# Kernel optimization log

Measured on AMD Instinct MI355X. Metric: run time of the kernel, lower is better.

The kernel has to match this reference:

```python
import jax, jax.numpy as jnp
import numpy as np

N_NODES = 4096
N_EDGES = 524288
IN_DIM = 6
EMB_N = 4
EMB_D = 8
EDGE_D = 1
HID = 64
N_HEADS = 4
LN_EPS = 1e-5


def _layernorm(h, g, b):
    m = jnp.mean(h, axis=-1, keepdims=True)
    v = jnp.mean(jnp.square(h - m), axis=-1, keepdims=True)
    return (h - m) * jax.lax.rsqrt(v + LN_EPS) * g + b


def setup_inputs() -> dict:
    key = jax.random.key(0)
    ks = jax.random.split(key, 16)
    s = lambda fan_in: 1.0 / np.sqrt(fan_in)
    inp = {
        'x': jax.random.normal(ks[0], (N_NODES, IN_DIM), jnp.float32),
        'edge_attr': jax.random.uniform(ks[1], (N_EDGES, EDGE_D), jnp.float32),
        'entity_emb': jax.random.normal(ks[2], (EMB_N, EMB_D), jnp.float32),
        'lin1_w': jax.random.uniform(ks[3], (HID, IN_DIM + EMB_D + EDGE_D), jnp.float32, -s(15), s(15)),
        'lin1_b': jnp.zeros((HID,), jnp.float32),
        'lay_w': jax.random.uniform(ks[4], (HID, HID), jnp.float32, -s(HID), s(HID)),
        'lay_b': jnp.zeros((HID,), jnp.float32),
        'ln_g': jnp.ones((HID,), jnp.float32),
        'ln_b': jnp.zeros((HID,), jnp.float32),
        'in_proj_w': jax.random.uniform(ks[5], (3 * HID, HID), jnp.float32, -s(HID), s(HID)),
        'in_proj_b': jnp.zeros((3 * HID,), jnp.float32),
        'out_proj_w': jax.random.uniform(ks[6], (HID, HID), jnp.float32, -s(HID), s(HID)),
        'out_proj_b': jnp.zeros((HID,), jnp.float32),
        'an_g': jnp.ones((HID,), jnp.float32),
        'an_b': jnp.zeros((HID,), jnp.float32),
        'out_w': jax.random.uniform(ks[7], (HID, HID), jnp.float32, -s(HID), s(HID)),
        'out_b': jnp.zeros((HID,), jnp.float32),
        'edge_index': jax.random.randint(ks[8], (2, N_EDGES), 0, N_NODES, jnp.int64),
        'entity_type': jax.random.randint(ks[9], (N_NODES,), 0, EMB_N, jnp.int64),
    }
    return inp


def reference(x, edge_attr, entity_emb, lin1_w, lin1_b, lay_w, lay_b, ln_g, ln_b,
              in_proj_w, in_proj_b, out_proj_w, out_proj_b, an_g, an_b, out_w, out_b,
              edge_index, entity_type):
    # --- EmbedConv ---
    # concat node features with entity embedding: [N, 6+8]
    xe = jnp.concatenate([x, entity_emb[entity_type]], axis=-1)
    src, dst = edge_index[0], edge_index[1]
    # gather source nodes + edge attr: [E, 15]
    msg = jnp.concatenate([xe[src], edge_attr], axis=-1)
    msg = _layernorm(jax.nn.relu(msg @ lin1_w.T + lin1_b), ln_g, ln_b)
    # layer_N = 1 extra layer, shared LayerNorm
    msg = _layernorm(jax.nn.relu(msg @ lay_w.T + lay_b), ln_g, ln_b)
    # scatter-add aggregate into destination nodes: [N, 64]
    h = jax.ops.segment_sum(msg, dst, num_segments=N_NODES)
    # --- MultiheadAttention over all nodes as one sequence (eval: no dropout) ---
    qkv = h @ in_proj_w.T + in_proj_b  # [N, 3H]
    q, k, v = jnp.split(qkv, 3, axis=-1)
    hd = HID // N_HEADS
    q = q.reshape(N_NODES, N_HEADS, hd).transpose(1, 0, 2)  # [h, n, d]
    k = k.reshape(N_NODES, N_HEADS, hd).transpose(1, 0, 2)
    v = v.reshape(N_NODES, N_HEADS, hd).transpose(1, 0, 2)
    scores = jnp.einsum('hnd,hmd->hnm', q, k) / np.sqrt(hd)
    attn = jax.nn.softmax(scores, axis=-1)
    o = jnp.einsum('hnm,hmd->hnd', attn, v).transpose(1, 0, 2).reshape(N_NODES, HID)
    o = o @ out_proj_w.T + out_proj_b
    h = _layernorm(h + o, an_g, an_b)
    # --- output layer ---
    return h @ out_w.T + out_b
```

## Files before the change

kernel.cpp:

```cpp
#include <hip/hip_runtime.h>

#define N_NODES 4096
#define N_EDGES 524288
#define HID 64

typedef short short8 __attribute__((ext_vector_type(8)));
typedef float f32x4 __attribute__((ext_vector_type(4)));

__device__ __forceinline__ float bcastf(float v, int l) {
    return __int_as_float(__builtin_amdgcn_readlane(__float_as_int(v), l));
}

__device__ __forceinline__ void wave_sum2(float& a, float& b) {
    #pragma unroll
    for (int off = 32; off > 0; off >>= 1) {
        a += __shfl_xor(a, off, 64);
        b += __shfl_xor(b, off, 64);
    }
}

__device__ __forceinline__ short f2bf(float f) {
    unsigned u = __float_as_uint(f);
    u = u + 0x7FFFu + ((u >> 16) & 1u);
    return (short)(u >> 16);
}
__device__ __forceinline__ float bf2f(short s) {
    return __uint_as_float(((unsigned)(unsigned short)s) << 16);
}
__device__ __forceinline__ void split_cheap(float f, short& hi, short& lo) {
    unsigned u = __float_as_uint(f);
    unsigned hb = u & 0xffff0000u;
    float lof = f - __uint_as_float(hb);
    hi = (short)(u >> 16);
    lo = (short)(__float_as_uint(lof) >> 16);
}

__global__ void xe_hist_wprep(const float* __restrict__ x, const float* __restrict__ emb,
                              const int* __restrict__ etype, const int* __restrict__ ei,
                              const float* __restrict__ w1, const float* __restrict__ w2,
                              const float* __restrict__ ipw,
                              unsigned short* __restrict__ xh, unsigned short* __restrict__ xl,
                              int* __restrict__ cnt, int* __restrict__ rank,
                              unsigned short* __restrict__ w1fh, unsigned short* __restrict__ w1fl,
                              unsigned short* __restrict__ w2fh, unsigned short* __restrict__ w2fl,
                              unsigned short* __restrict__ ipfh, unsigned short* __restrict__ ipfl) {
    int tid = blockIdx.x * 256 + threadIdx.x;
    int d = ei[N_EDGES + tid];
    rank[tid] = atomicAdd(&cnt[d], 1);
    if (tid < N_NODES * 16) {
        int n = tid >> 4, i = tid & 15;
        float v = 0.f;
        if (i < 6) v = x[n * 6 + i];
        else if (i < 14) v = emb[etype[n] * 8 + (i - 6)];
        short hi = f2bf(v);
        short lo = f2bf(v - bf2f(hi));
        xh[tid] = (unsigned short)hi;
        xl[tid] = (unsigned short)lo;
    }
    if (tid < 2048) {
        int g = tid >> 9, ln = (tid >> 3) & 63, j = tid & 7;
        int mm = ln & 15, qq = ln >> 4;
        int k = qq * 8 + j;
        float w = (k < 15) ? w1[(g * 16 + mm) * 15 + k] : 0.f;
        short hi = f2bf(w);
        w1fh[tid] = (unsigned short)hi;
        w1fl[tid] = (unsigned short)f2bf(w - bf2f(hi));
    }
    if (tid < 4096) {
        int idx = tid >> 9, ln = (tid >> 3) & 63, j = tid & 7;
        int mm = ln & 15, qq = ln >> 4;
        int g = idx >> 1, tt = idx & 1;
        float w = w2[(g * 16 + mm) * 64 + tt * 32 + qq * 8 + j];
        short hi = f2bf(w);
        w2fh[tid] = (unsigned short)hi;
        w2fl[tid] = (unsigned short)f2bf(w - bf2f(hi));
    }
    if (tid < 12288) {
        int idx = tid >> 9, ln = (tid >> 3) & 63, j = tid & 7;
        int mm = ln & 15, qq = ln >> 4;
        int og = idx >> 1, tt = idx & 1;
        float w = ipw[(og * 16 + mm) * 64 + tt * 32 + qq * 8 + j];
        short hi = f2bf(w);
        ipfh[tid] = (unsigned short)hi;
        ipfl[tid] = (unsigned short)f2bf(w - bf2f(hi));
    }
}

__global__ void __launch_bounds__(256) scatter_scan(
        const int* __restrict__ cnt, const int* __restrict__ ei,
        const float* __restrict__ edge_attr, const int* __restrict__ rank,
        int* __restrict__ bnd,
        int* __restrict__ ssrc, float* __restrict__ sea) {
    __shared__ int lbnd[4096];
    __shared__ int wsum[4];
    int t = threadIdx.x;
    int base = t * 16;
    int v16[16];
    int T = 0;
    #pragma unroll
    for (int j = 0; j < 16; j++) { v16[j] = cnt[base + j]; T += v16[j]; }
    int inc = T;
    int l = t & 63;
    #pragma unroll
    for (int off = 1; off < 64; off <<= 1) {
        int v = __shfl_up(inc, off, 64);
        if (l >= off) inc += v;
    }
    if (l == 63) wsum[t >> 6] = inc;
    __syncthreads();
    int wo = 0;
    for (int w = 0; w < (t >> 6); w++) wo += wsum[w];
    int run = wo + inc - T;
    #pragma unroll
    for (int j = 0; j < 16; j++) {
        lbnd[base + j] = run;
        run += v16[j];
    }
    if (blockIdx.x == 0) {
        #pragma unroll
        for (int j = 0; j < 16; j++) bnd[base + j] = lbnd[base + j];
        if (t == 255) bnd[4096] = run;
    }
    __syncthreads();
    int e = blockIdx.x * 256 + t;
    int d = ei[N_EDGES + e];
    int pos = lbnd[d] + rank[e];
    ssrc[pos] = ei[e];
    sea[pos] = edge_attr[e];
}

__global__ void __launch_bounds__(256) edge_gather_mfma(
        const unsigned short* __restrict__ xh, const unsigned short* __restrict__ xl,
        const int* __restrict__ ssrc, const float* __restrict__ sea,
        const int* __restrict__ bnd,
        const unsigned short* __restrict__ w1fh, const unsigned short* __restrict__ w1fl,
        const unsigned short* __restrict__ w2fh, const unsigned short* __restrict__ w2fl,
        const float* __restrict__ w1, const float* __restrict__ b1,
        const float* __restrict__ b2,
        const float* __restrict__ lg, const float* __restrict__ lb,
        float* __restrict__ h) {
    __shared__ float Y[4][16 * 68];
    __shared__ float hpart[4][64];
    int lane = threadIdx.x & 63;
    int wv = threadIdx.x >> 6;
    int m = lane & 15;
    int q = lane >> 4;
    float* Yw = Y[wv];

    short8 b1h[4], b1l[4], b2h[8], b2l[8];
    #pragma unroll
    for (int g = 0; g < 4; g++) {
        b1h[g] = *(const short8*)(w1fh + (g * 64 + lane) * 8);
        b1l[g] = *(const short8*)(w1fl + (g * 64 + lane) * 8);
    }
    #pragma unroll
    for (int idx = 0; idx < 8; idx++) {
        b2h[idx] = *(const short8*)(w2fh + (idx * 64 + lane) * 8);
        b2l[idx] = *(const short8*)(w2fl + (idx * 64 + lane) * 8);
    }
    float w14[4], b1v[4], b2v[4], gam[4], bet[4];
    #pragma unroll
    for (int g = 0; g < 4; g++) {
        int row = g * 16 + m;
        w14[g] = w1[row * 15 + 14];
        b1v[g] = b1[row];
        b2v[g] = b2[row];
        gam[g] = lg[row];
        bet[g] = lb[row];
    }

    int node = blockIdx.x * 2 + (wv >> 1);
    int hf = wv & 1;
    int start = bnd[node], end = bnd[node + 1];
    int ntiles = (end - start + 15) >> 4;
    int h0 = (ntiles + 1) >> 1;
    int tcnt = hf ? (ntiles - h0) : h0;
    int astart = start + (hf ? h0 : 0) * 16;
    float acc[4] = {0.f, 0.f, 0.f, 0.f};

    for (int t = 0; t < tcnt; t++) {
        int base = astart + t * 16;
        int e = base + m;
        int srcn = ssrc[(e < end) ? e : (end - 1)];
        short8 a1h = (short8)0, a1l = (short8)0;
        if (q < 2) {
            a1h = *(const short8*)(xh + srcn * 16 + q * 8);
            a1l = *(const short8*)(xl + srcn * 16 + q * 8);
        }
        float ea[4];
        #pragma unroll
        for (int i = 0; i < 4; i++) {
            int idx = base + q * 4 + i;
            ea[i] = (idx < end) ? sea[idx] : 0.f;
        }
        f32x4 c1[4];
        #pragma unroll
        for (int g = 0; g < 4; g++) {
            f32x4 c = {0.f, 0.f, 0.f, 0.f};
            c = __builtin_amdgcn_mfma_f32_16x16x32_bf16(a1l, b1h[g], c, 0, 0, 0);
            c = __builtin_amdgcn_mfma_f32_16x16x32_bf16(a1h, b1l[g], c, 0, 0, 0);
            c = __builtin_amdgcn_mfma_f32_16x16x32_bf16(a1h, b1h[g], c, 0, 0, 0);
            c1[g] = c;
        }
        float s[4] = {0, 0, 0, 0}, s2[4] = {0, 0, 0, 0};
        float t1[4][4];
        #pragma unroll
        for (int g = 0; g < 4; g++) {
            #pragma unroll
            for (int i = 0; i < 4; i++) {
                float v = c1[g][i] + b1v[g] + w14[g] * ea[i];
                v = fmaxf(v, 0.f);
                t1[g][i] = v;
                s[i] += v;
                s2[i] += v * v;
            }
        }
        #pragma unroll
        for (int off = 1; off < 16; off <<= 1) {
            #pragma unroll
            for (int i = 0; i < 4; i++) {
                s[i] += __shfl_xor(s[i], off, 64);
                s2[i] += __shfl_xor(s2[i], off, 64);
            }
        }
        #pragma unroll
        for (int i = 0; i < 4; i++) {
            float mean = s[i] * (1.f / 64.f);
            float var = s2[i] * (1.f / 64.f) - mean * mean;
            s[i] = mean;
            s2[i] = rsqrtf(var + 1e-5f);
        }
        #pragma unroll
        for (int g = 0; g < 4; g++) {
            #pragma unroll
            for (int i = 0; i < 4; i++) {
                float y = (t1[g][i] - s[i]) * s2[i] * gam[g] + bet[g];
                Yw[(q * 4 + i) * 68 + g * 16 + m] = y;
            }
        }
        short8 a2h[2], a2l[2];
        #pragma unroll
        for (int t2 = 0; t2 < 2; t2++) {
            #pragma unroll
            for (int j = 0; j < 8; j++) {
                float v = Yw[m * 68 + t2 * 32 + q * 8 + j];
                short hi, lo;
                split_cheap(v, hi, lo);
                a2h[t2][j] = hi;
                a2l[t2][j] = lo;
            }
        }
        float s_[4] = {0, 0, 0, 0}, s2_[4] = {0, 0, 0, 0};
        float t2v[4][4];
        #pragma unroll
        for (int g = 0; g < 4; g++) {
            f32x4 c = {0.f, 0.f, 0.f, 0.f};
            #pragma unroll
            for (int t2 = 0; t2 < 2; t2++) {
                c = __builtin_amdgcn_mfma_f32_16x16x32_bf16(a2l[t2], b2h[g * 2 + t2], c, 0, 0, 0);
                c = __builtin_amdgcn_mfma_f32_16x16x32_bf16(a2h[t2], b2l[g * 2 + t2], c, 0, 0, 0);
                c = __builtin_amdgcn_mfma_f32_16x16x32_bf16(a2h[t2], b2h[g * 2 + t2], c, 0, 0, 0);
            }
            #pragma unroll
            for (int i = 0; i < 4; i++) {
                float v = c[i] + b2v[g];
                v = fmaxf(v, 0.f);
                t2v[g][i] = v;
                s_[i] += v;
                s2_[i] += v * v;
            }
        }
        #pragma unroll
        for (int off = 1; off < 16; off <<= 1) {
            #pragma unroll
            for (int i = 0; i < 4; i++) {
                s_[i] += __shfl_xor(s_[i], off, 64);
                s2_[i] += __shfl_xor(s2_[i], off, 64);
            }
        }
        #pragma unroll
        for (int i = 0; i < 4; i++) {
            float mean = s_[i] * (1.f / 64.f);
            float var = s2_[i] * (1.f / 64.f) - mean * mean;
            float rs = rsqrtf(var + 1e-5f);
            bool valid = (base + q * 4 + i) < end;
            #pragma unroll
            for (int g = 0; g < 4; g++) {
                float z = (t2v[g][i] - mean) * rs * gam[g] + bet[g];
                if (valid) acc[g] += z;
            }
        }
    }
    #pragma unroll
    for (int g = 0; g < 4; g++) {
        acc[g] += __shfl_xor(acc[g], 16, 64);
        acc[g] += __shfl_xor(acc[g], 32, 64);
    }
    float a01 = (q & 1) ? acc[1] : acc[0];
    float a23 = (q & 1) ? acc[3] : acc[2];
    float av = (q & 2) ? a23 : a01;
    hpart[wv][q * 16 + m] = av;
    __syncthreads();
    if (threadIdx.x < 128) {
        int nn = threadIdx.x >> 6, f = threadIdx.x & 63;
        h[(blockIdx.x * 2 + nn) * 64 + f] = hpart[2 * nn][f] + hpart[2 * nn + 1][f];
    }
}

__global__ void __launch_bounds__(256) qkv_mfma(
        const float* __restrict__ h, const float* __restrict__ b,
        const unsigned short* __restrict__ ipfh, const unsigned short* __restrict__ ipfl,
        unsigned short* __restrict__ qhp, unsigned short* __restrict__ qlp,
        unsigned short* __restrict__ khp, unsigned short* __restrict__ klp,
        unsigned short* __restrict__ vT) {
    int lane = threadIdx.x & 63;
    int wv = threadIdx.x >> 6;
    int m = lane & 15;
    int q = lane >> 4;
    int wid = blockIdx.x * 4 + wv;
    int tile = wid / 12;
    int og = wid - tile * 12;
    short8 bh[2], bl[2];
    #pragma unroll
    for (int t = 0; t < 2; t++) {
        bh[t] = *(const short8*)(ipfh + ((og * 2 + t) * 64 + lane) * 8);
        bl[t] = *(const short8*)(ipfl + ((og * 2 + t) * 64 + lane) * 8);
    }
    f32x4 c = {0.f, 0.f, 0.f, 0.f};
    #pragma unroll
    for (int t = 0; t < 2; t++) {
        const float* hr = h + (tile * 16 + m) * 64 + t * 32 + q * 8;
        float4 f0 = *(const float4*)hr;
        float4 f1 = *(const float4*)(hr + 4);
        float av8[8] = {f0.x, f0.y, f0.z, f0.w, f1.x, f1.y, f1.z, f1.w};
        short8 ah, al;
        #pragma unroll
        for (int j = 0; j < 8; j++) {
            short hi, lo;
            split_cheap(av8[j], hi, lo);
            ah[j] = hi;
            al[j] = lo;
        }
        c = __builtin_amdgcn_mfma_f32_16x16x32_bf16(al, bh[t], c, 0, 0, 0);
        c = __builtin_amdgcn_mfma_f32_16x16x32_bf16(ah, bl[t], c, 0, 0, 0);
        c = __builtin_amdgcn_mfma_f32_16x16x32_bf16(ah, bh[t], c, 0, 0, 0);
    }
    int o = og * 16 + m;
    float bias = b[o];
    #pragma unroll
    for (int r = 0; r < 4; r++) {
        int node = tile * 16 + q * 4 + r;
        float val = c[r] + bias;
        if (og < 4) {
            float aq = val * (0.25f * 1.44269504f);
            size_t idx = ((size_t)(og * N_NODES + node)) * 16 + m;
            short hi = f2bf(aq);
            qhp[idx] = (unsigned short)hi;
            qlp[idx] = (unsigned short)f2bf(aq - bf2f(hi));
        } else if (og < 8) {
            size_t idx = ((size_t)((og - 4) * N_NODES + node)) * 16 + m;
            short hi = f2bf(val);
            khp[idx] = (unsigned short)hi;
            klp[idx] = (unsigned short)f2bf(val - bf2f(hi));
        } else {
            int feat = (og - 8) * 16 + m;
            vT[(size_t)feat * N_NODES + node] = (unsigned short)f2bf(val);
        }
    }
}

__global__ void __launch_bounds__(256) attn_mfma(
        const unsigned short* __restrict__ qhp, const unsigned short* __restrict__ qlp,
        const unsigned short* __restrict__ khp, const unsigned short* __restrict__ klp,
        const unsigned short* __restrict__ vT,
        float* __restrict__ part_o, float* __restrict__ part_ml) {
    __shared__ unsigned short Pl[4][16 * 72];
    int lane = threadIdx.x & 63;
    int wv = threadIdx.x >> 6;
    int m = lane & 15;
    int g = lane >> 4;
    unsigned short* Pw = Pl[wv];
    const short8 vones = {0x3F80, 0x3F80, 0x3F80, 0x3F80, 0x3F80, 0x3F80, 0x3F80, 0x3F80};

    int wid = blockIdx.x * 4 + wv;
    int kc = wid & 7;
    int qt = (wid >> 3) & 255;
    int head = wid >> 11;

    short8 aqh = (short8)0, aql = (short8)0;
    if (g < 2) {
        size_t qi = ((size_t)(head * N_NODES + qt * 16 + m)) * 16 + g * 8;
        aqh = *(const short8*)(qhp + qi);
        aql = *(const short8*)(qlp + qi);
    }
    float mS[4], lS[4];
    #pragma unroll
    for (int r = 0; r < 4; r++) { mS[r] = -3e38f; lS[r] = 0.f; }
    f32x4 Ot = {0.f, 0.f, 0.f, 0.f};

    const unsigned short* khb = khp + (size_t)head * N_NODES * 16;
    const unsigned short* klb = klp + (size_t)head * N_NODES * 16;
    const unsigned short* vtb = vT + (size_t)(head * 16 + m) * N_NODES;

    for (int bblk = 0; bblk < 8; bblk++) {
        int n0 = kc * 512 + bblk * 64;
        f32x4 S[4];
        #pragma unroll
        for (int s = 0; s < 4; s++) {
            short8 bkh = (short8)0, bkl = (short8)0;
            if (g < 2) {
                size_t ki = ((size_t)(n0 + s * 16 + m)) * 16 + g * 8;
                bkh = *(const short8*)(khb + ki);
                bkl = *(const short8*)(klb + ki);
            }
            f32x4 c = {0.f, 0.f, 0.f, 0.f};
            c = __builtin_amdgcn_mfma_f32_16x16x32_bf16(aqh, bkl, c, 0, 0, 0);
            c = __builtin_amdgcn_mfma_f32_16x16x32_bf16(aql, bkh, c, 0, 0, 0);
            c = __builtin_amdgcn_mfma_f32_16x16x32_bf16(aqh, bkh, c, 0, 0, 0);
            S[s] = c;
        }
        float mr[4];
        #pragma unroll
        for (int r = 0; r < 4; r++)
            mr[r] = fmaxf(fmaxf(S[0][r], S[1][r]), fmaxf(S[2][r], S[3][r]));
        #pragma unroll
        for (int off = 1; off < 16; off <<= 1)
            #pragma unroll
            for (int r = 0; r < 4; r++) mr[r] = fmaxf(mr[r], __shfl_xor(mr[r], off, 64));
        float alpha[4];
        #pragma unroll
        for (int r = 0; r < 4; r++) {
            float mn = fmaxf(mS[r], mr[r]);
            alpha[r] = exp2f(mS[r] - mn);
            mS[r] = mn;
        }
        #pragma unroll
        for (int s = 0; s < 4; s++) {
            #pragma unroll
            for (int r = 0; r < 4; r++) {
                float p = exp2f(S[s][r] - mS[r]);
                Pw[(g * 4 + r) * 72 + s * 16 + m] = (unsigned short)f2bf(p);
            }
        }
        #pragma unroll
        for (int r = 0; r < 4; r++) lS[r] *= alpha[r];
        int sel = lane & 3;
        float a01 = (sel & 1) ? alpha[1] : alpha[0];
        float a23 = (sel & 1) ? alpha[3] : alpha[2];
        float aown = (sel & 2) ? a23 : a01;
        int srcl = ((m >> 2) << 4) | (m & 3);
        float ab = __int_as_float(__builtin_amdgcn_ds_bpermute(srcl << 2, __float_as_int(aown)));
        #pragma unroll
        for (int r = 0; r < 4; r++) Ot[r] *= ab;
        f32x4 cl = {0.f, 0.f, 0.f, 0.f};
        #pragma unroll
        for (int t = 0; t < 2; t++) {
            short8 avf = *(const short8*)(vtb + n0 + t * 32 + g * 8);
            short8 bpf = *(const short8*)(Pw + m * 72 + t * 32 + g * 8);
            cl = __builtin_amdgcn_mfma_f32_16x16x32_bf16(vones, bpf, cl, 0, 0, 0);
            Ot = __builtin_amdgcn_mfma_f32_16x16x32_bf16(avf, bpf, Ot, 0, 0, 0);
        }
        #pragma unroll
        for (int r = 0; r < 4; r++) {
            float rsum = __int_as_float(
                __builtin_amdgcn_ds_bpermute((g * 4 + r) << 2, __float_as_int(cl[0])));
            lS[r] += rsum;
        }
    }
    size_t pb = ((size_t)(head * 8 + kc) * 256 + qt) * 256;
    *(f32x4*)(part_o + pb + m * 16 + g * 4) = Ot;
    if (m == 0) {
        size_t mb = ((size_t)(head * 8 + kc) * 256 + qt) * 32;
        #pragma unroll
        for (int r = 0; r < 4; r++) {
            part_ml[mb + g * 4 + r] = mS[r];
            part_ml[mb + 16 + g * 4 + r] = lS[r];
        }
    }
}

__global__ void post_kernel(const float* __restrict__ h,
                            const float* __restrict__ part_o, const float* __restrict__ part_ml,
                            const float* __restrict__ opw, const float* __restrict__ opb,
                            const float* __restrict__ ag, const float* __restrict__ ab,
                            const float* __restrict__ ow, const float* __restrict__ ob,
                            float* __restrict__ out) {
    __shared__ float wl1[64 * 65];
    __shared__ float wl2[64 * 65];
    for (int i = threadIdx.x; i < 4096; i += blockDim.x) {
        int r = i >> 6, c = i & 63;
        wl1[r * 65 + c] = opw[i];
        wl2[r * 65 + c] = ow[i];
    }
    __syncthreads();
    int lane = threadIdx.x & 63;
    int n = blockIdx.x * 4 + (threadIdx.x >> 6);
    int j = lane;
    int head = j >> 4, d = j & 15;
    int qt = n >> 4, qi = n & 15;
    float M = -3e38f, L = 0.f, Ov = 0.f;
    #pragma unroll
    for (int c = 0; c < 8; c++) {
        size_t base = ((size_t)(head * 8 + c) * 256 + qt);
        float mc = part_ml[base * 32 + qi];
        float lc = part_ml[base * 32 + 16 + qi];
        float ov = part_o[base * 256 + qi * 16 + d];
        if (mc > M) {
            float sc = exp2f(M - mc);
            M = mc;
            L = L * sc + lc;
            Ov = Ov * sc + ov;
        } else {
            float sc = exp2f(mc - M);
            L = fmaf(lc, sc, L);
            Ov = fmaf(ov, sc, Ov);
        }
    }
    float oj = Ov / L;
    float acc = opb[j];
    #pragma unroll
    for (int k = 0; k < 64; k++) acc = fmaf(wl1[j * 65 + k], bcastf(oj, k), acc);
    float r = h[n * 64 + j] + acc;
    float s = r, s2 = r * r;
    wave_sum2(s, s2);
    float mean = s * (1.f / 64.f);
    float var = s2 * (1.f / 64.f) - mean * mean;
    float hn = (r - mean) * rsqrtf(var + 1e-5f) * ag[j] + ab[j];
    float acc2 = ob[j];
    #pragma unroll
    for (int k = 0; k < 64; k++) acc2 = fmaf(wl2[j * 65 + k], bcastf(hn, k), acc2);
    out[n * 64 + j] = acc2;
}

extern "C" void kernel_launch(void* const* d_in, const int* in_sizes, int n_in,
                              void* d_out, int out_size, void* d_ws, size_t ws_size,
                              hipStream_t stream) {
    const float* x        = (const float*)d_in[0];
    const float* edge_attr= (const float*)d_in[1];
    const float* emb      = (const float*)d_in[2];
    const float* lin1_w   = (const float*)d_in[3];
    const float* lin1_b   = (const float*)d_in[4];
    const float* lay_w    = (const float*)d_in[5];
    const float* lay_b    = (const float*)d_in[6];
    const float* ln_g     = (const float*)d_in[7];
    const float* ln_b     = (const float*)d_in[8];
    const float* ipw      = (const float*)d_in[9];
    const float* ipb      = (const float*)d_in[10];
    const float* opw      = (const float*)d_in[11];
    const float* opb      = (const float*)d_in[12];
    const float* ang      = (const float*)d_in[13];
    const float* anb      = (const float*)d_in[14];
    const float* ow       = (const float*)d_in[15];
    const float* ob       = (const float*)d_in[16];
    const int*   ei       = (const int*)d_in[17];
    const int*   et       = (const int*)d_in[18];

    char* wsb = (char*)d_ws;
    size_t off = 0;
    unsigned short* xe_hi = (unsigned short*)(wsb + off); off += 131072;
    unsigned short* xe_lo = (unsigned short*)(wsb + off); off += 131072;
    float* h              = (float*)(wsb + off);          off += 1048576;
    unsigned short* qhp   = (unsigned short*)(wsb + off); off += 524288;
    unsigned short* qlp   = (unsigned short*)(wsb + off); off += 524288;
    unsigned short* khp   = (unsigned short*)(wsb + off); off += 524288;
    unsigned short* klp   = (unsigned short*)(wsb + off); off += 524288;
    unsigned short* vT    = (unsigned short*)(wsb + off); off += 524288;
    float* part_o         = (float*)(wsb + off);          off += 8388608;
    float* part_ml        = (float*)(wsb + off);          off += 1048576;
    int*   cnt            = (int*)(wsb + off);            off += 16384;
    int*   bnd            = (int*)(wsb + off);            off += 16388;
    off = (off + 255) & ~(size_t)255;
    int*   rank           = (int*)(wsb + off);            off += 2097152;
    int*   ssrc           = (int*)(wsb + off);            off += 2097152;
    float* sea            = (float*)(wsb + off);          off += 2097152;
    unsigned short* w1fh  = (unsigned short*)(wsb + off); off += 4096;
    unsigned short* w1fl  = (unsigned short*)(wsb + off); off += 4096;
    unsigned short* w2fh  = (unsigned short*)(wsb + off); off += 8192;
    unsigned short* w2fl  = (unsigned short*)(wsb + off); off += 8192;
    unsigned short* ipfh  = (unsigned short*)(wsb + off); off += 24576;
    unsigned short* ipfl  = (unsigned short*)(wsb + off); off += 24576;

    (void)hipMemsetAsync(cnt, 0, 4096 * sizeof(int), stream);
    xe_hist_wprep<<<2048, 256, 0, stream>>>(x, emb, et, ei, lin1_w, lay_w, ipw,
                                            xe_hi, xe_lo, cnt, rank,
                                            w1fh, w1fl, w2fh, w2fl, ipfh, ipfl);
    scatter_scan<<<2048, 256, 0, stream>>>(cnt, ei, edge_attr, rank, bnd, ssrc, sea);
    edge_gather_mfma<<<2048, 256, 0, stream>>>(xe_hi, xe_lo, ssrc, sea, bnd,
                                               w1fh, w1fl, w2fh, w2fl,
                                               lin1_w, lin1_b, lay_b, ln_g, ln_b, h);
    qkv_mfma<<<768, 256, 0, stream>>>(h, ipb, ipfh, ipfl, qhp, qlp, khp, klp, vT);
    attn_mfma<<<2048, 256, 0, stream>>>(qhp, qlp, khp, klp, vT, part_o, part_ml);
    post_kernel<<<1024, 256, 0, stream>>>(h, part_o, part_ml, opw, opb, ang, anb, ow, ob,
                                          (float*)d_out);
}
```

Measured before the change: 270.5 us.

## Precompute per-node first-layer projection and fold LayerNorm affine into weights

The first linear layer's node-dependent part (x and entity embedding times lin1_w plus bias) is computed once per node into a float table A1. The per-edge kernel now only gathers that row, adds the edge-attr term and applies relu and LayerNorm in registers, removing the first MFMA stage and the LDS round-trip. LayerNorm gamma/beta are folded into the second-layer weights and bias, and the final gamma/beta are applied once per node after aggregation using the edge count. Each block now handles one node with four waves striding tiles, and the second-layer weights are staged in LDS. The cost is a larger per-edge gather (64 floats instead of 32 bf16 values) and fp32 rounding that differs slightly from the reference.

New measurement: 242.2 us. 1.12x faster.

```diff
diff --git a/kernel.cpp b/kernel.cpp
--- a/kernel.cpp
+++ b/kernel.cpp
@@ -35,42 +35,36 @@
     lo = (short)(__float_as_uint(lof) >> 16);
 }
 
-__global__ void xe_hist_wprep(const float* __restrict__ x, const float* __restrict__ emb,
-                              const int* __restrict__ etype, const int* __restrict__ ei,
-                              const float* __restrict__ w1, const float* __restrict__ w2,
-                              const float* __restrict__ ipw,
-                              unsigned short* __restrict__ xh, unsigned short* __restrict__ xl,
-                              int* __restrict__ cnt, int* __restrict__ rank,
-                              unsigned short* __restrict__ w1fh, unsigned short* __restrict__ w1fl,
-                              unsigned short* __restrict__ w2fh, unsigned short* __restrict__ w2fl,
-                              unsigned short* __restrict__ ipfh, unsigned short* __restrict__ ipfl) {
+__global__ void hist_prep(const float* __restrict__ x, const float* __restrict__ emb,
+                          const int* __restrict__ etype, const int* __restrict__ ei,
+                          const float* __restrict__ w1, const float* __restrict__ b1,
+                          const float* __restrict__ w2, const float* __restrict__ lng,
+                          const float* __restrict__ lnb, const float* __restrict__ b2,
+                          const float* __restrict__ ipw,
+                          float* __restrict__ A1, int* __restrict__ cnt, int* __restrict__ rank,
+                          unsigned short* __restrict__ w2fh, unsigned short* __restrict__ w2fl,
+                          unsigned short* __restrict__ ipfh, unsigned short* __restrict__ ipfl,
+                          float* __restrict__ b2p) {
     int tid = blockIdx.x * 256 + threadIdx.x;
     int d = ei[N_EDGES + tid];
     rank[tid] = atomicAdd(&cnt[d], 1);
-    if (tid < N_NODES * 16) {
-        int n = tid >> 4, i = tid & 15;
-        float v = 0.f;
-        if (i < 6) v = x[n * 6 + i];
-        else if (i < 14) v = emb[etype[n] * 8 + (i - 6)];
-        short hi = f2bf(v);
-        short lo = f2bf(v - bf2f(hi));
-        xh[tid] = (unsigned short)hi;
-        xl[tid] = (unsigned short)lo;
-    }
-    if (tid < 2048) {
-        int g = tid >> 9, ln = (tid >> 3) & 63, j = tid & 7;
-        int mm = ln & 15, qq = ln >> 4;
-        int k = qq * 8 + j;
-        float w = (k < 15) ? w1[(g * 16 + mm) * 15 + k] : 0.f;
-        short hi = f2bf(w);
-        w1fh[tid] = (unsigned short)hi;
-        w1fl[tid] = (unsigned short)f2bf(w - bf2f(hi));
+    if (tid < N_NODES * 64) {
+        int n = tid >> 6, f = tid & 63;
+        const float* wr = w1 + f * 15;
+        float acc = b1[f];
+        #pragma unroll
+        for (int k = 0; k < 6; k++) acc = fmaf(x[n * 6 + k], wr[k], acc);
+        int e = etype[n];
+        #pragma unroll
+        for (int k = 0; k < 8; k++) acc = fmaf(emb[e * 8 + k], wr[6 + k], acc);
+        A1[tid] = acc;
     }
     if (tid < 4096) {
         int idx = tid >> 9, ln = (tid >> 3) & 63, j = tid & 7;
         int mm = ln & 15, qq = ln >> 4;
         int g = idx >> 1, tt = idx & 1;
-        float w = w2[(g * 16 + mm) * 64 + tt * 32 + qq * 8 + j];
+        int col = tt * 32 + qq * 8 + j;
+        float w = w2[(g * 16 + mm) * 64 + col] * lng[col];
         short hi = f2bf(w);
         w2fh[tid] = (unsigned short)hi;
         w2fl[tid] = (unsigned short)f2bf(w - bf2f(hi));
@@ -83,6 +77,11 @@
         short hi = f2bf(w);
         ipfh[tid] = (unsigned short)hi;
         ipfl[tid] = (unsigned short)f2bf(w - bf2f(hi));
+    }
+    if (tid < 64) {
+        float acc = b2[tid];
+        for (int c = 0; c < 64; c++) acc = fmaf(w2[tid * 64 + c], lnb[c], acc);
+        b2p[tid] = acc;
     }
 }
 
@@ -129,164 +128,125 @@
     sea[pos] = edge_attr[e];
 }
 
-__global__ void __launch_bounds__(256) edge_gather_mfma(
-        const unsigned short* __restrict__ xh, const unsigned short* __restrict__ xl,
+__global__ void __launch_bounds__(256, 4) edge_gather_mfma(
+        const float* __restrict__ A1,
         const int* __restrict__ ssrc, const float* __restrict__ sea,
         const int* __restrict__ bnd,
-        const unsigned short* __restrict__ w1fh, const unsigned short* __restrict__ w1fl,
         const unsigned short* __restrict__ w2fh, const unsigned short* __restrict__ w2fl,
-        const float* __restrict__ w1, const float* __restrict__ b1,
-        const float* __restrict__ b2,
+        const float* __restrict__ w1, const float* __restrict__ b2p,
         const float* __restrict__ lg, const float* __restrict__ lb,
         float* __restrict__ h) {
-    __shared__ float Y[4][16 * 68];
+    __shared__ uint4 lw2h4[512];
+    __shared__ uint4 lw2l4[512];
     __shared__ float hpart[4][64];
-    int lane = threadIdx.x & 63;
-    int wv = threadIdx.x >> 6;
+    int tid = threadIdx.x;
+    {
+        const uint4* gh = (const uint4*)w2fh;
+        const uint4* gl = (const uint4*)w2fl;
+        lw2h4[tid] = gh[tid];
+        lw2h4[tid + 256] = gh[tid + 256];
+        lw2l4[tid] = gl[tid];
+        lw2l4[tid + 256] = gl[tid + 256];
+    }
+    const unsigned short* lw2h = (const unsigned short*)lw2h4;
+    const unsigned short* lw2l = (const unsigned short*)lw2l4;
+
+    int lane = tid & 63;
+    int wv = tid >> 6;
     int m = lane & 15;
     int q = lane >> 4;
-    float* Yw = Y[wv];
-
-    short8 b1h[4], b1l[4], b2h[8], b2l[8];
-    #pragma unroll
-    for (int g = 0; g < 4; g++) {
-        b1h[g] = *(const short8*)(w1fh + (g * 64 + lane) * 8);
-        b1l[g] = *(const short8*)(w1fl + (g * 64 + lane) * 8);
-    }
-    #pragma unroll
-    for (int idx = 0; idx < 8; idx++) {
-        b2h[idx] = *(const short8*)(w2fh + (idx * 64 + lane) * 8);
-        b2l[idx] = *(const short8*)(w2fl + (idx * 64 + lane) * 8);
-    }
-    float w14[4], b1v[4], b2v[4], gam[4], bet[4];
-    #pragma unroll
-    for (int g = 0; g < 4; g++) {
-        int row = g * 16 + m;
-        w14[g] = w1[row * 15 + 14];
-        b1v[g] = b1[row];
-        b2v[g] = b2[row];
-        gam[g] = lg[row];
-        bet[g] = lb[row];
-    }
-
-    int node = blockIdx.x * 2 + (wv >> 1);
-    int hf = wv & 1;
+
+    float w14f[16];
+    #pragma unroll
+    for (int t2 = 0; t2 < 2; t2++)
+        #pragma unroll
+        for (int j = 0; j < 8; j++)
+            w14f[t2 * 8 + j] = w1[(t2 * 32 + q * 8 + j) * 15 + 14];
+    float b2v[4];
+    #pragma unroll
+    for (int g = 0; g < 4; g++) b2v[g] = b2p[g * 16 + m];
+
+    int node = blockIdx.x;
     int start = bnd[node], end = bnd[node + 1];
     int ntiles = (end - start + 15) >> 4;
-    int h0 = (ntiles + 1) >> 1;
-    int tcnt = hf ? (ntiles - h0) : h0;
-    int astart = start + (hf ? h0 : 0) * 16;
     float acc[4] = {0.f, 0.f, 0.f, 0.f};
-
-    for (int t = 0; t < tcnt; t++) {
-        int base = astart + t * 16;
+    __syncthreads();
+
+    for (int t = wv; t < ntiles; t += 4) {
+        int base = start + t * 16;
         int e = base + m;
-        int srcn = ssrc[(e < end) ? e : (end - 1)];
-        short8 a1h = (short8)0, a1l = (short8)0;
-        if (q < 2) {
-            a1h = *(const short8*)(xh + srcn * 16 + q * 8);
-            a1l = *(const short8*)(xl + srcn * 16 + q * 8);
-        }
-        float ea[4];
-        #pragma unroll
-        for (int i = 0; i < 4; i++) {
-            int idx = base + q * 4 + i;
-            ea[i] = (idx < end) ? sea[idx] : 0.f;
-        }
-        f32x4 c1[4];
+        int ec = (e < end) ? e : (end - 1);
+        int srcn = ssrc[ec];
+        float eav = sea[ec];
+        const float* ar = A1 + srcn * 64 + q * 8;
+        float4 va = *(const float4*)(ar);
+        float4 vb = *(const float4*)(ar + 4);
+        float4 vc = *(const float4*)(ar + 32);
+        float4 vd = *(const float4*)(ar + 36);
+        float v[16] = {va.x, va.y, va.z, va.w, vb.x, vb.y, vb.z, vb.w,
+                       vc.x, vc.y, vc.z, vc.w, vd.x, vd.y, vd.z, vd.w};
+        float s = 0.f, s2 = 0.f;
+        #pragma unroll
+        for (int j = 0; j < 16; j++) {
+            float u = fmaxf(fmaf(w14f[j], eav, v[j]), 0.f);
+            v[j] = u;
+            s += u;
+            s2 = fmaf(u, u, s2);
+        }
+        s += __shfl_xor(s, 16, 64);  s2 += __shfl_xor(s2, 16, 64);
+        s += __shfl_xor(s, 32, 64);  s2 += __shfl_xor(s2, 32, 64);
+        float mean = s * (1.f / 64.f);
+        float var = s2 * (1.f / 64.f) - mean * mean;
+        float rs = rsqrtf(var + 1e-5f);
+        float a0 = -mean * rs;
+        short8 a2h[2], a2l[2];
+        #pragma unroll
+        for (int t2 = 0; t2 < 2; t2++)
+            #pragma unroll
+            for (int j = 0; j < 8; j++) {
+                short hi, lo;
+                split_cheap(fmaf(v[t2 * 8 + j], rs, a0), hi, lo);
+                a2h[t2][j] = hi;
+                a2l[t2][j] = lo;
+            }
+        int ob = (t >> 20);
+        float s_[4] = {0, 0, 0, 0}, s2_[4] = {0, 0, 0, 0};
+        float t2v[4][4];
         #pragma unroll
         for (int g = 0; g < 4; g++) {
             f32x4 c = {0.f, 0.f, 0.f, 0.f};
-            c = __builtin_amdgcn_mfma_f32_16x16x32_bf16(a1l, b1h[g], c, 0, 0, 0);
-            c = __builtin_amdgcn_mfma_f32_16x16x32_bf16(a1h, b1l[g], c, 0, 0, 0);
-            c = __builtin_amdgcn_mfma_f32_16x16x32_bf16(a1h, b1h[g], c, 0, 0, 0);
-            c1[g] = c;
-        }
-        float s[4] = {0, 0, 0, 0}, s2[4] = {0, 0, 0, 0};
-        float t1[4][4];
-        #pragma unroll
-        for (int g = 0; g < 4; g++) {
+            #pragma unroll
+            for (int t2 = 0; t2 < 2; t2++) {
+                short8 bh = *(const short8*)(lw2h + ((g * 2 + t2) * 64 + lane + ob) * 8);
+                short8 bl = *(const short8*)(lw2l + ((g * 2 + t2) * 64 + lane + ob) * 8);
+                c = __builtin_amdgcn_mfma_f32_16x16x32_bf16(a2l[t2], bh, c, 0, 0, 0);
+                c = __builtin_amdgcn_mfma_f32_16x16x32_bf16(a2h[t2], bl, c, 0, 0, 0);
+                c = __builtin_amdgcn_mfma_f32_16x16x32_bf16(a2h[t2], bh, c, 0, 0, 0);
+            }
             #pragma unroll
             for (int i = 0; i < 4; i++) {
-                float v = c1[g][i] + b1v[g] + w14[g] * ea[i];
-                v = fmaxf(v, 0.f);
-                t1[g][i] = v;
-                s[i] += v;
-                s2[i] += v * v;
-            }
-        }
-        #pragma unroll
-        for (int off = 1; off < 16; off <<= 1) {
-            #pragma unroll
-            for (int i = 0; i < 4; i++) {
-                s[i] += __shfl_xor(s[i], off, 64);
-                s2[i] += __shfl_xor(s2[i], off, 64);
-            }
-        }
-        #pragma unroll
-        for (int i = 0; i < 4; i++) {
-            float mean = s[i] * (1.f / 64.f);
-            float var = s2[i] * (1.f / 64.f) - mean * mean;
-            s[i] = mean;
-            s2[i] = rsqrtf(var + 1e-5f);
-        }
-        #pragma unroll
-        for (int g = 0; g < 4; g++) {
-            #pragma unroll
-            for (int i = 0; i < 4; i++) {
-                float y = (t1[g][i] - s[i]) * s2[i] * gam[g] + bet[g];
-                Yw[(q * 4 + i) * 68 + g * 16 + m] = y;
-            }
-        }
-        short8 a2h[2], a2l[2];
-        #pragma unroll
-        for (int t2 = 0; t2 < 2; t2++) {
-            #pragma unroll
-            for (int j = 0; j < 8; j++) {
-                float v = Yw[m * 68 + t2 * 32 + q * 8 + j];
-                short hi, lo;
-                split_cheap(v, hi, lo);
-                a2h[t2][j] = hi;
-                a2l[t2][j] = lo;
-            }
-        }
-        float s_[4] = {0, 0, 0, 0}, s2_[4] = {0, 0, 0, 0};
-        float t2v[4][4];
-        #pragma unroll
-        for (int g = 0; g < 4; g++) {
-            f32x4 c = {0.f, 0.f, 0.f, 0.f};
-            #pragma unroll
-            for (int t2 = 0; t2 < 2; t2++) {
-                c = __builtin_amdgcn_mfma_f32_16x16x32_bf16(a2l[t2], b2h[g * 2 + t2], c, 0, 0, 0);
-                c = __builtin_amdgcn_mfma_f32_16x16x32_bf16(a2h[t2], b2l[g * 2 + t2], c, 0, 0, 0);
-                c = __builtin_amdgcn_mfma_f32_16x16x32_bf16(a2h[t2], b2h[g * 2 + t2], c, 0, 0, 0);
-            }
-            #pragma unroll
-            for (int i = 0; i < 4; i++) {
-                float v = c[i] + b2v[g];
-                v = fmaxf(v, 0.f);
-                t2v[g][i] = v;
-                s_[i] += v;
-                s2_[i] += v * v;
-            }
-        }
-        #pragma unroll
-        for (int off = 1; off < 16; off <<= 1) {
+                float vv = fmaxf(c[i] + b2v[g], 0.f);
+                t2v[g][i] = vv;
+                s_[i] += vv;
+                s2_[i] = fmaf(vv, vv, s2_[i]);
+            }
+        }
+        #pragma unroll
+        for (int off = 1; off < 16; off <<= 1)
             #pragma unroll
             for (int i = 0; i < 4; i++) {
                 s_[i] += __shfl_xor(s_[i], off, 64);
                 s2_[i] += __shfl_xor(s2_[i], off, 64);
             }
-        }
         #pragma unroll
         for (int i = 0; i < 4; i++) {
-            float mean = s_[i] * (1.f / 64.f);
-            float var = s2_[i] * (1.f / 64.f) - mean * mean;
-            float rs = rsqrtf(var + 1e-5f);
+            float mean2 = s_[i] * (1.f / 64.f);
+            float var2 = s2_[i] * (1.f / 64.f) - mean2 * mean2;
+            float rs2 = rsqrtf(var2 + 1e-5f);
             bool valid = (base + q * 4 + i) < end;
             #pragma unroll
             for (int g = 0; g < 4; g++) {
-                float z = (t2v[g][i] - mean) * rs * gam[g] + bet[g];
+                float z = (t2v[g][i] - mean2) * rs2;
                 if (valid) acc[g] += z;
             }
         }
@@ -301,9 +261,9 @@
     float av = (q & 2) ? a23 : a01;
     hpart[wv][q * 16 + m] = av;
     __syncthreads();
-    if (threadIdx.x < 128) {
-        int nn = threadIdx.x >> 6, f = threadIdx.x & 63;
-        h[(blockIdx.x * 2 + nn) * 64 + f] = hpart[2 * nn][f] + hpart[2 * nn + 1][f];
+    if (tid < 64) {
+        float sum = hpart[0][tid] + hpart[1][tid] + hpart[2][tid] + hpart[3][tid];
+        h[node * 64 + tid] = lg[tid] * sum + (float)(end - start) * lb[tid];
     }
 }
 
@@ -557,8 +517,7 @@
 
     char* wsb = (char*)d_ws;
     size_t off = 0;
-    unsigned short* xe_hi = (unsigned short*)(wsb + off); off += 131072;
-    unsigned short* xe_lo = (unsigned short*)(wsb + off); off += 131072;
+    float* A1             = (float*)(wsb + off);          off += 1048576;
     float* h              = (float*)(wsb + off);          off += 1048576;
     unsigned short* qhp   = (unsigned short*)(wsb + off); off += 524288;
     unsigned short* qlp   = (unsigned short*)(wsb + off); off += 524288;
@@ -573,21 +532,18 @@
     int*   rank           = (int*)(wsb + off);            off += 2097152;
     int*   ssrc           = (int*)(wsb + off);            off += 2097152;
     float* sea            = (float*)(wsb + off);          off += 2097152;
-    unsigned short* w1fh  = (unsigned short*)(wsb + off); off += 4096;
-    unsigned short* w1fl  = (unsigned short*)(wsb + off); off += 4096;
     unsigned short* w2fh  = (unsigned short*)(wsb + off); off += 8192;
     unsigned short* w2fl  = (unsigned short*)(wsb + off); off += 8192;
     unsigned short* ipfh  = (unsigned short*)(wsb + off); off += 24576;
     unsigned short* ipfl  = (unsigned short*)(wsb + off); off += 24576;
+    float* b2p            = (float*)(wsb + off);          off += 256;
 
     (void)hipMemsetAsync(cnt, 0, 4096 * sizeof(int), stream);
-    xe_hist_wprep<<<2048, 256, 0, stream>>>(x, emb, et, ei, lin1_w, lay_w, ipw,
-                                            xe_hi, xe_lo, cnt, rank,
-                                            w1fh, w1fl, w2fh, w2fl, ipfh, ipfl);
+    hist_prep<<<2048, 256, 0, stream>>>(x, emb, et, ei, lin1_w, lin1_b, lay_w, ln_g, ln_b,
+                                        lay_b, ipw, A1, cnt, rank, w2fh, w2fl, ipfh, ipfl, b2p);
     scatter_scan<<<2048, 256, 0, stream>>>(cnt, ei, edge_attr, rank, bnd, ssrc, sea);
-    edge_gather_mfma<<<2048, 256, 0, stream>>>(xe_hi, xe_lo, ssrc, sea, bnd,
-                                               w1fh, w1fl, w2fh, w2fl,
-                                               lin1_w, lin1_b, lay_b, ln_g, ln_b, h);
+    edge_gather_mfma<<<4096, 256, 0, stream>>>(A1, ssrc, sea, bnd, w2fh, w2fl,
+                                               lin1_w, b2p, ln_g, ln_b, h);
     qkv_mfma<<<768, 256, 0, stream>>>(h, ipb, ipfh, ipfl, qhp, qlp, khp, klp, vT);
     attn_mfma<<<2048, 256, 0, stream>>>(qhp, qlp, khp, klp, vT, part_o, part_ml);
     post_kernel<<<1024, 256, 0, stream>>>(h, part_o, part_ml, opw, opb, ang, anb, ow, ob,
```
